# Optimization experiments

Measured on AMD Instinct MI355X. Metric: run time of the kernel, lower is better.

Reference implementation:

```python
import jax, jax.numpy as jnp
import numpy as np
from jax import lax

B, H, W = 4096, 15, 15
P, V = 16, 32
D = P + V            # 48
PCODE = 2380
NEMB = 2 * (PCODE + 1)  # 4762


def _conv(x, w, b=None, groups=1, pad='SAME'):
    # x: [B,C,H,W], w: [O, I/groups, kh, kw] (torch OIHW layout)
    y = lax.conv_general_dilated(
        x, w, window_strides=(1, 1), padding=pad,
        dimension_numbers=('NCHW', 'OIHW', 'NCHW'),
        feature_group_count=groups)
    if b is not None:
        y = y + b[None, :, None, None]
    return y


def setup_inputs() -> dict:
    key = jax.random.key(0)
    ks = jax.random.split(key, 18)
    f = lambda k, shape: (jax.random.normal(k, shape, jnp.float32) * 0.05)
    inp = {
        'emb': f(ks[0], (NEMB, D)),
        'conv_w': f(ks[1], (D, 1, 3, 3)),      # depthwise, groups=D
        'conv_b': f(ks[2], (D,)),
        'ppw_w': f(ks[3], (P, P, 1, 1)),
        'ppw_b': f(ks[4], (P,)),
        'pdw_w': f(ks[5], (P, 1, 3, 3)),       # depthwise, groups=P
        'pdw_b': f(ks[6], (P,)),
        'pf_w': f(ks[7], (1, P, 1, 1)),        # final policy conv, no bias
        'vpw_w': f(ks[8], (V, V, 1, 1)),
        'vpw_b': f(ks[9], (V,)),
        'vl1_w': f(ks[10], (V, V)),
        'vl1_b': f(ks[11], (V,)),
        'vl2_w': f(ks[12], (V, V)),
        'vl2_b': f(ks[13], (V,)),
        'vf_w': f(ks[14], (3, V)),
        'vf_b': f(ks[15], (3,)),
        'sparse_feature_input': jax.random.randint(ks[16], (B, 12, H, W), 0, PCODE, jnp.int32),
        'board_input': jax.random.randint(ks[17], (B, 2, H, W), 0, 2, jnp.int32),
    }
    return inp


def reference(emb, conv_w, conv_b, ppw_w, ppw_b, pdw_w, pdw_b, pf_w,
              vpw_w, vpw_b, vl1_w, vl1_b, vl2_w, vl2_b, vf_w, vf_b,
              sparse_feature_input, board_input):
    relu = jax.nn.relu
    # --- PatternCodeEmbedding ---
    pcode = sparse_feature_input[:, 10:12]                     # [B,2,H,W]
    pcode = jnp.where(board_input > 0, PCODE, pcode)
    pcode = pcode + jnp.array([0, PCODE + 1], jnp.int32)[None, :, None, None]
    feat = emb[pcode].sum(axis=1)                              # [B,H,W,D]
    feat = jnp.transpose(feat, (0, 3, 1, 2))                   # [B,D,H,W]
    # --- trunk depthwise conv ---
    feat = relu(_conv(feat, conv_w, conv_b, groups=D))
    # --- policy head ---
    pol = feat[:, :P]
    pol = relu(_conv(pol, ppw_w, ppw_b))
    pol = relu(_conv(pol, pdw_w, pdw_b, groups=P))
    pol = _conv(pol, pf_w)                                     # [B,1,H,W]
    # --- value head ---
    val = feat[:, P:]
    val = relu(_conv(val, vpw_w, vpw_b))
    val = jnp.mean(val, axis=(2, 3))                           # [B,V]
    val = relu(val @ vl1_w.T + vl1_b)
    val = relu(val @ vl2_w.T + vl2_b)
    val = val @ vf_w.T + vf_b                                  # [B,3]
    return val, pol
```

## Files before the change

kernel.cpp:

```cpp
#include <hip/hip_runtime.h>
#include <hip/hip_fp16.h>

typedef _Float16 half8  __attribute__((ext_vector_type(8)));
typedef _Float16 half4_t __attribute__((ext_vector_type(4)));
typedef _Float16 half2_t __attribute__((ext_vector_type(2)));
typedef float f32x4 __attribute__((ext_vector_type(4)));

namespace {
constexpr int NT = 256;
constexpr int NPIX = 225;
constexpr int PCODE_C = 2380;

constexpr int OFF_A     = 0;
constexpr int OFF_X     = 25200;
constexpr int OFF_WC    = 48240;
constexpr int OFF_WCB   = 49104;
constexpr int OFF_WPD   = 49200;
constexpr int OFF_WPDB  = 49488;
constexpr int OFF_SV    = 49520;
constexpr int OFF_H1    = 49648;
constexpr int OFF_H2    = 49776;
constexpr int SMEM_BYTES = 49904;

constexpr int OFF_POLA  = 0;
constexpr int OFF_POLB  = 10800;
}

__device__ __forceinline__ void wave_fence() {
    asm volatile("s_waitcnt lgkmcnt(0)" ::: "memory");
}

__global__ __launch_bounds__(NT) void patnet_kernel(
    const float* __restrict__ emb,
    const float* __restrict__ conv_w, const float* __restrict__ conv_b,
    const float* __restrict__ ppw_w,  const float* __restrict__ ppw_b,
    const float* __restrict__ pdw_w,  const float* __restrict__ pdw_b,
    const float* __restrict__ pf_w,
    const float* __restrict__ vpw_w,  const float* __restrict__ vpw_b,
    const float* __restrict__ vl1_w,  const float* __restrict__ vl1_b,
    const float* __restrict__ vl2_w,  const float* __restrict__ vl2_b,
    const float* __restrict__ vf_w,   const float* __restrict__ vf_b,
    const int* __restrict__ sparse,   const int* __restrict__ board,
    float* __restrict__ out, int batch)
{
    __shared__ __align__(16) unsigned char smem[SMEM_BYTES];
    const int tid  = threadIdx.x;
    const int b    = blockIdx.x;
    const int lane = tid & 63;
    const int wave = tid >> 6;

    int c0 = 0, c1 = 0;
    if (tid < NPIX) {
        int s10 = sparse[b * 2700 + 10 * NPIX + tid];
        int s11 = sparse[b * 2700 + 11 * NPIX + tid];
        int b0  = board[b * 450 + tid];
        int b1  = board[b * 450 + NPIX + tid];
        c0 = (b0 > 0) ? PCODE_C : s10;
        c1 = ((b1 > 0) ? PCODE_C : s11) + (PCODE_C + 1);
    }

    {
        _Float16* Wc   = (_Float16*)(smem + OFF_WC);
        _Float16* Wcb  = (_Float16*)(smem + OFF_WCB);
        _Float16* Wpd  = (_Float16*)(smem + OFF_WPD);
        _Float16* Wpdb = (_Float16*)(smem + OFF_WPDB);
        for (int i = tid; i < 432; i += NT) {
            int cg = i / 72, rem = i - cg * 72;
            int t = rem >> 3, j = rem & 7;
            Wc[i] = (_Float16)conv_w[(cg * 8 + j) * 9 + t];
        }
        for (int i = tid; i < 48; i += NT) Wcb[i] = (_Float16)conv_b[i];
        for (int i = tid; i < 144; i += NT) {
            int cg = i / 72, rem = i - cg * 72;
            int t = rem >> 3, j = rem & 7;
            Wpd[i] = (_Float16)pdw_w[(cg * 8 + j) * 9 + t];
        }
        for (int i = tid; i < 16; i += NT) Wpdb[i] = (_Float16)pdw_b[i];
    }

    if (tid < NPIX) {
        const float* e0 = emb + c0 * 48;
        const float* e1 = emb + c1 * 48;
        #pragma unroll
        for (int g = 0; g < 6; g++) {
            f32x4 x0 = *(const f32x4*)(e0 + g * 8);
            f32x4 x1 = *(const f32x4*)(e0 + g * 8 + 4);
            f32x4 y0 = *(const f32x4*)(e1 + g * 8);
            f32x4 y1 = *(const f32x4*)(e1 + g * 8 + 4);
            f32x4 s0 = x0 + y0, s1 = x1 + y1;
            half8 hv = {(_Float16)s0.x, (_Float16)s0.y, (_Float16)s0.z, (_Float16)s0.w,
                        (_Float16)s1.x, (_Float16)s1.y, (_Float16)s1.z, (_Float16)s1.w};
            *(half8*)(smem + OFF_A + tid * 112 + g * 16) = hv;
        }
    }
    __syncthreads();

    if (tid < 252) {
        int cg = tid % 6, prow = tid / 6;
        const _Float16* wb = (const _Float16*)(smem + OFF_WC) + cg * 72;
        half8 wv[9];
        #pragma unroll
        for (int t = 0; t < 9; t++) wv[t] = *(const half8*)(wb + t * 8);
        half8 bias = *(const half8*)((const _Float16*)(smem + OFF_WCB) + cg * 8);
        for (int p = prow; p < NPIX; p += 42) {
            int y = p / 15, x = p - y * 15;
            half8 acc = bias;
            #pragma unroll
            for (int dy = -1; dy <= 1; dy++) {
                int yy = y + dy;
                if ((unsigned)yy >= 15u) continue;
                #pragma unroll
                for (int dx = -1; dx <= 1; dx++) {
                    int xx = x + dx;
                    if ((unsigned)xx >= 15u) continue;
                    half8 v = *(const half8*)(smem + OFF_A + (yy * 15 + xx) * 112 + cg * 16);
                    acc = __builtin_elementwise_fma(v, wv[(dy + 1) * 3 + (dx + 1)], acc);
                }
            }
            acc = __builtin_elementwise_max(acc, (half8)(_Float16)0.f);
            *(half8*)(smem + OFF_X + p * 96 + cg * 16) = acc;
        }
    }
    __syncthreads();

    const int n = lane & 15, q = lane >> 4;

    if (wave < 3) {
        half8 af;
        {
            const float* wp = ppw_w + n * 16 + (q & 1) * 8;
            f32x4 w0 = *(const f32x4*)wp;
            f32x4 w1 = *(const f32x4*)(wp + 4);
            half8 t = {(_Float16)w0.x, (_Float16)w0.y, (_Float16)w0.z, (_Float16)w0.w,
                       (_Float16)w1.x, (_Float16)w1.y, (_Float16)w1.z, (_Float16)w1.w};
            af = (q < 2) ? t : (half8)(_Float16)0.f;
        }
        f32x4 pb = *(const f32x4*)(ppw_b + q * 4);
        const int tlo = (wave == 0) ? 0 : ((wave == 1) ? 3 : 8);
        const int thi = (wave == 0) ? 6 : ((wave == 1) ? 11 : 15);
        for (int t = tlo; t < thi; t++) {
            int p = t * 16 + n;
            half8 bf = *(const half8*)(smem + OFF_X + p * 96 + q * 16);
            f32x4 d = __builtin_amdgcn_mfma_f32_16x16x32_f16(af, bf, (f32x4)(0.f), 0, 0, 0);
            if (p < NPIX) {
                half4_t hv = {(_Float16)fmaxf(d.x + pb.x, 0.f),
                              (_Float16)fmaxf(d.y + pb.y, 0.f),
                              (_Float16)fmaxf(d.z + pb.z, 0.f),
                              (_Float16)fmaxf(d.w + pb.w, 0.f)};
                *(half4_t*)(smem + OFF_POLA + p * 48 + q * 8) = hv;
            }
        }
        wave_fence();

        const int px0 = wave * 75;
        {
            int cg = lane & 1;
            const _Float16* wb = (const _Float16*)(smem + OFF_WPD) + cg * 72;
            half8 wv[9];
            #pragma unroll
            for (int t = 0; t < 9; t++) wv[t] = *(const half8*)(wb + t * 8);
            half8 bias = *(const half8*)((const _Float16*)(smem + OFF_WPDB) + cg * 8);
            for (int i = 0; i < 3; i++) {
                int idx = i * 64 + lane;
                if (idx < 150) {
                    int px = px0 + (idx >> 1);
                    int y = px / 15, x = px - y * 15;
                    half8 acc = bias;
                    #pragma unroll
                    for (int dy = -1; dy <= 1; dy++) {
                        int yy = y + dy;
                        if ((unsigned)yy >= 15u) continue;
                        #pragma unroll
                        for (int dx = -1; dx <= 1; dx++) {
                            int xx = x + dx;
                            if ((unsigned)xx >= 15u) continue;
                            half8 v = *(const half8*)(smem + OFF_POLA + (yy * 15 + xx) * 48 + cg * 16);
                            acc = __builtin_elementwise_fma(v, wv[(dy + 1) * 3 + (dx + 1)], acc);
                        }
                    }
                    acc = __builtin_elementwise_max(acc, (half8)(_Float16)0.f);
                    *(half8*)(smem + OFF_POLB + px * 32 + cg * 16) = acc;
                }
            }
        }
        wave_fence();

        {
            half2_t pf[8];
            #pragma unroll
            for (int j = 0; j < 8; j++)
                pf[j] = half2_t{(_Float16)pf_w[2 * j], (_Float16)pf_w[2 * j + 1]};
            for (int i = 0; i < 2; i++) {
                int off = i * 64 + lane;
                if (off < 75) {
                    int px = px0 + off;
                    half8 u0 = *(const half8*)(smem + OFF_POLB + px * 32);
                    half8 u1 = *(const half8*)(smem + OFF_POLB + px * 32 + 16);
                    float acc = 0.f;
                    acc = __builtin_amdgcn_fdot2(half2_t{u0[0], u0[1]}, pf[0], acc, false);
                    acc = __builtin_amdgcn_fdot2(half2_t{u0[2], u0[3]}, pf[1], acc, false);
                    acc = __builtin_amdgcn_fdot2(half2_t{u0[4], u0[5]}, pf[2], acc, false);
                    acc = __builtin_amdgcn_fdot2(half2_t{u0[6], u0[7]}, pf[3], acc, false);
                    acc = __builtin_amdgcn_fdot2(half2_t{u1[0], u1[1]}, pf[4], acc, false);
                    acc = __builtin_amdgcn_fdot2(half2_t{u1[2], u1[3]}, pf[5], acc, false);
                    acc = __builtin_amdgcn_fdot2(half2_t{u1[4], u1[5]}, pf[6], acc, false);
                    acc = __builtin_amdgcn_fdot2(half2_t{u1[6], u1[7]}, pf[7], acc, false);
                    out[3 * batch + b * NPIX + px] = acc;
                }
            }
        }
    } else {
        half8 af0, af1;
        {
            const float* wp = vpw_w + n * 32 + q * 8;
            f32x4 w0 = *(const f32x4*)wp, w1 = *(const f32x4*)(wp + 4);
            af0 = half8{(_Float16)w0.x, (_Float16)w0.y, (_Float16)w0.z, (_Float16)w0.w,
                        (_Float16)w1.x, (_Float16)w1.y, (_Float16)w1.z, (_Float16)w1.w};
            const float* wp2 = vpw_w + (16 + n) * 32 + q * 8;
            f32x4 v0 = *(const f32x4*)wp2, v1 = *(const f32x4*)(wp2 + 4);
            af1 = half8{(_Float16)v0.x, (_Float16)v0.y, (_Float16)v0.z, (_Float16)v0.w,
                        (_Float16)v1.x, (_Float16)v1.y, (_Float16)v1.z, (_Float16)v1.w};
        }
        f32x4 vb0 = *(const f32x4*)(vpw_b + q * 4);
        f32x4 vb1 = *(const f32x4*)(vpw_b + 16 + q * 4);
        f32x4 a0 = {0.f, 0.f, 0.f, 0.f}, a1 = {0.f, 0.f, 0.f, 0.f};
        for (int t = 0; t < 15; t++) {
            int p = t * 16 + n;
            half8 bf = *(const half8*)(smem + OFF_X + p * 96 + 32 + q * 16);
            f32x4 d0 = __builtin_amdgcn_mfma_f32_16x16x32_f16(af0, bf, (f32x4)(0.f), 0, 0, 0);
            f32x4 d1 = __builtin_amdgcn_mfma_f32_16x16x32_f16(af1, bf, (f32x4)(0.f), 0, 0, 0);
            if (p < NPIX) {
                #pragma unroll
                for (int r = 0; r < 4; r++) {
                    a0[r] += fmaxf(d0[r] + vb0[r], 0.f);
                    a1[r] += fmaxf(d1[r] + vb1[r], 0.f);
                }
            }
        }
        #pragma unroll
        for (int s = 1; s < 16; s <<= 1) {
            #pragma unroll
            for (int r = 0; r < 4; r++) {
                a0[r] += __shfl_xor(a0[r], s, 64);
                a1[r] += __shfl_xor(a1[r], s, 64);
            }
        }
        if (n == 0) {
            f32x4 m0 = a0 * (1.f / 225.f), m1 = a1 * (1.f / 225.f);
            *(f32x4*)(smem + OFF_SV + q * 16) = m0;
            *(f32x4*)(smem + OFF_SV + 64 + q * 16) = m1;
        }
        wave_fence();

        int o = lane & 31;
        float acc1 = vl1_b[o];
        #pragma unroll
        for (int g = 0; g < 8; g++) {
            f32x4 sv = *(const f32x4*)(smem + OFF_SV + g * 16);
            f32x4 w4 = *(const f32x4*)(vl1_w + o * 32 + g * 4);
            acc1 += sv.x * w4.x + sv.y * w4.y + sv.z * w4.z + sv.w * w4.w;
        }
        acc1 = fmaxf(acc1, 0.f);
        if (lane < 32) *(float*)(smem + OFF_H1 + o * 4) = acc1;
        wave_fence();

        float acc2 = vl2_b[o];
        #pragma unroll
        for (int g = 0; g < 8; g++) {
            f32x4 hv = *(const f32x4*)(smem + OFF_H1 + g * 16);
            f32x4 w4 = *(const f32x4*)(vl2_w + o * 32 + g * 4);
            acc2 += hv.x * w4.x + hv.y * w4.y + hv.z * w4.z + hv.w * w4.w;
        }
        acc2 = fmaxf(acc2, 0.f);
        if (lane < 32) *(float*)(smem + OFF_H2 + o * 4) = acc2;
        wave_fence();

        if (lane < 3) {
            float acc3 = vf_b[lane];
            #pragma unroll
            for (int g = 0; g < 8; g++) {
                f32x4 hv = *(const f32x4*)(smem + OFF_H2 + g * 16);
                f32x4 w4 = *(const f32x4*)(vf_w + lane * 32 + g * 4);
                acc3 += hv.x * w4.x + hv.y * w4.y + hv.z * w4.z + hv.w * w4.w;
            }
            out[b * 3 + lane] = acc3;
        }
    }
}

extern "C" void kernel_launch(void* const* d_in, const int* in_sizes, int n_in,
                              void* d_out, int out_size, void* d_ws, size_t ws_size,
                              hipStream_t stream) {
    const float* emb    = (const float*)d_in[0];
    const float* conv_w = (const float*)d_in[1];
    const float* conv_b = (const float*)d_in[2];
    const float* ppw_w  = (const float*)d_in[3];
    const float* ppw_b  = (const float*)d_in[4];
    const float* pdw_w  = (const float*)d_in[5];
    const float* pdw_b  = (const float*)d_in[6];
    const float* pf_w   = (const float*)d_in[7];
    const float* vpw_w  = (const float*)d_in[8];
    const float* vpw_b  = (const float*)d_in[9];
    const float* vl1_w  = (const float*)d_in[10];
    const float* vl1_b  = (const float*)d_in[11];
    const float* vl2_w  = (const float*)d_in[12];
    const float* vl2_b  = (const float*)d_in[13];
    const float* vf_w   = (const float*)d_in[14];
    const float* vf_b   = (const float*)d_in[15];
    const int* sparse   = (const int*)d_in[16];
    const int* board    = (const int*)d_in[17];
    float* out = (float*)d_out;

    int batch = in_sizes[16] / 2700;
    patnet_kernel<<<batch, NT, 0, stream>>>(
        emb, conv_w, conv_b, ppw_w, ppw_b, pdw_w, pdw_b, pf_w,
        vpw_w, vpw_b, vl1_w, vl1_b, vl2_w, vl2_b, vf_w, vf_b,
        sparse, board, out, batch);
}
```

Before: 178.4 us.

## Use zero-padded channel-group-major LDS layout and strip-based depthwise convolutions

```diff
diff --git a/kernel.cpp b/kernel.cpp
--- a/kernel.cpp
+++ b/kernel.cpp
@@ -4,6 +4,7 @@
 typedef _Float16 half8  __attribute__((ext_vector_type(8)));
 typedef _Float16 half4_t __attribute__((ext_vector_type(4)));
 typedef _Float16 half2_t __attribute__((ext_vector_type(2)));
+typedef __fp16   fp16x2  __attribute__((ext_vector_type(2)));
 typedef float f32x4 __attribute__((ext_vector_type(4)));
 
 namespace {
@@ -11,26 +12,31 @@
 constexpr int NPIX = 225;
 constexpr int PCODE_C = 2380;
 
+constexpr int APITCH_Y  = 272;
+constexpr int APITCH_CG = 4624;
+
 constexpr int OFF_A     = 0;
-constexpr int OFF_X     = 25200;
-constexpr int OFF_WC    = 48240;
-constexpr int OFF_WCB   = 49104;
-constexpr int OFF_WPD   = 49200;
-constexpr int OFF_WPDB  = 49488;
-constexpr int OFF_SV    = 49520;
-constexpr int OFF_H1    = 49648;
-constexpr int OFF_H2    = 49776;
-constexpr int SMEM_BYTES = 49904;
+constexpr int OFF_X     = 27744;
+constexpr int OFF_WC    = 50784;
+constexpr int OFF_WCB   = 51648;
+constexpr int OFF_WPD   = 51744;
+constexpr int OFF_WPDB  = 52032;
+constexpr int OFF_SV    = 52064;
+constexpr int OFF_H1    = 52192;
+constexpr int OFF_H2    = 52320;
+constexpr int SMEM_BYTES = 52448;
 
 constexpr int OFF_POLA  = 0;
-constexpr int OFF_POLB  = 10800;
-}
-
+}
+
+__device__ __forceinline__ half2_t pkrtz(float a, float b) {
+    return __builtin_bit_cast(half2_t, __builtin_amdgcn_cvt_pkrtz(a, b));
+}
 __device__ __forceinline__ void wave_fence() {
     asm volatile("s_waitcnt lgkmcnt(0)" ::: "memory");
 }
 
-__global__ __launch_bounds__(NT) void patnet_kernel(
+__global__ __launch_bounds__(NT, 3) void patnet_kernel(
     const float* __restrict__ emb,
     const float* __restrict__ conv_w, const float* __restrict__ conv_b,
     const float* __restrict__ ppw_w,  const float* __restrict__ ppw_b,
@@ -76,11 +82,21 @@
             Wpd[i] = (_Float16)pdw_w[(cg * 8 + j) * 9 + t];
         }
         for (int i = tid; i < 16; i += NT) Wpdb[i] = (_Float16)pdw_b[i];
+        for (int i = tid; i < 384; i += NT) {
+            int cg = i >> 6, j = i & 63;
+            int row, col;
+            if (j < 17)      { row = 0;  col = j; }
+            else if (j < 34) { row = 16; col = j - 17; }
+            else { int k = j - 34; row = 1 + (k >> 1); col = (k & 1) * 16; }
+            *(half8*)(smem + OFF_A + cg * APITCH_CG + row * APITCH_Y + col * 16) = (half8)(_Float16)0.f;
+        }
     }
 
     if (tid < NPIX) {
         const float* e0 = emb + c0 * 48;
         const float* e1 = emb + c1 * 48;
+        int y = tid / 15, x = tid - y * 15;
+        unsigned char* abase = smem + OFF_A + (y + 1) * APITCH_Y + (x + 1) * 16;
         #pragma unroll
         for (int g = 0; g < 6; g++) {
             f32x4 x0 = *(const f32x4*)(e0 + g * 8);
@@ -88,141 +104,138 @@
             f32x4 y0 = *(const f32x4*)(e1 + g * 8);
             f32x4 y1 = *(const f32x4*)(e1 + g * 8 + 4);
             f32x4 s0 = x0 + y0, s1 = x1 + y1;
-            half8 hv = {(_Float16)s0.x, (_Float16)s0.y, (_Float16)s0.z, (_Float16)s0.w,
-                        (_Float16)s1.x, (_Float16)s1.y, (_Float16)s1.z, (_Float16)s1.w};
-            *(half8*)(smem + OFF_A + tid * 112 + g * 16) = hv;
+            half2_t q0 = pkrtz(s0.x, s0.y), q1 = pkrtz(s0.z, s0.w);
+            half2_t q2 = pkrtz(s1.x, s1.y), q3 = pkrtz(s1.z, s1.w);
+            half8 hv = {q0[0], q0[1], q1[0], q1[1], q2[0], q2[1], q3[0], q3[1]};
+            *(half8*)(abase + g * APITCH_CG) = hv;
         }
     }
     __syncthreads();
 
-    if (tid < 252) {
-        int cg = tid % 6, prow = tid / 6;
-        const _Float16* wb = (const _Float16*)(smem + OFF_WC) + cg * 72;
+    auto do_strip = [&](int t) {
+        int cg = t / 45, rem = t - cg * 45;
+        int y = rem / 3, s = rem - y * 3;
+        int xs = s * 5;
+        const unsigned char* wb = smem + OFF_WC + cg * 144;
         half8 wv[9];
         #pragma unroll
-        for (int t = 0; t < 9; t++) wv[t] = *(const half8*)(wb + t * 8);
-        half8 bias = *(const half8*)((const _Float16*)(smem + OFF_WCB) + cg * 8);
-        for (int p = prow; p < NPIX; p += 42) {
-            int y = p / 15, x = p - y * 15;
-            half8 acc = bias;
+        for (int i = 0; i < 9; i++) wv[i] = *(const half8*)(wb + i * 16);
+        half8 bias = *(const half8*)(smem + OFF_WCB + cg * 16);
+        half8 acc[5] = {bias, bias, bias, bias, bias};
+        const unsigned char* ab = smem + OFF_A + cg * APITCH_CG + y * APITCH_Y + xs * 16;
+        #pragma unroll
+        for (int c = 0; c < 7; c++) {
+            half8 v0 = *(const half8*)(ab + c * 16);
+            half8 v1 = *(const half8*)(ab + APITCH_Y + c * 16);
+            half8 v2 = *(const half8*)(ab + 2 * APITCH_Y + c * 16);
             #pragma unroll
-            for (int dy = -1; dy <= 1; dy++) {
-                int yy = y + dy;
-                if ((unsigned)yy >= 15u) continue;
-                #pragma unroll
-                for (int dx = -1; dx <= 1; dx++) {
-                    int xx = x + dx;
-                    if ((unsigned)xx >= 15u) continue;
-                    half8 v = *(const half8*)(smem + OFF_A + (yy * 15 + xx) * 112 + cg * 16);
-                    acc = __builtin_elementwise_fma(v, wv[(dy + 1) * 3 + (dx + 1)], acc);
+            for (int o = 0; o < 5; o++) {
+                int kx = c - o;
+                if (kx >= 0 && kx <= 2) {
+                    acc[o] = __builtin_elementwise_fma(v0, wv[kx],     acc[o]);
+                    acc[o] = __builtin_elementwise_fma(v1, wv[3 + kx], acc[o]);
+                    acc[o] = __builtin_elementwise_fma(v2, wv[6 + kx], acc[o]);
                 }
             }
-            acc = __builtin_elementwise_max(acc, (half8)(_Float16)0.f);
-            *(half8*)(smem + OFF_X + p * 96 + cg * 16) = acc;
-        }
-    }
+        }
+        unsigned char* xw = smem + OFF_X + (y * 15 + xs) * 96 + cg * 16;
+        #pragma unroll
+        for (int o = 0; o < 5; o++)
+            *(half8*)(xw + o * 96) = __builtin_elementwise_max(acc[o], (half8)(_Float16)0.f);
+    };
+    do_strip(tid);
+    {
+        int e = wave * 4 + lane;
+        if (lane < 4 && e < 14) do_strip(256 + e);
+    }
+
+    const int n = lane & 15, q = lane >> 4;
+    half8 af_p;
+    {
+        const float* wp = ppw_w + n * 16 + (q & 1) * 8;
+        f32x4 w0 = *(const f32x4*)wp, w1 = *(const f32x4*)(wp + 4);
+        half8 t = {(_Float16)w0.x, (_Float16)w0.y, (_Float16)w0.z, (_Float16)w0.w,
+                   (_Float16)w1.x, (_Float16)w1.y, (_Float16)w1.z, (_Float16)w1.w};
+        af_p = (q < 2) ? t : (half8)(_Float16)0.f;
+    }
+    f32x4 pb = *(const f32x4*)(ppw_b + q * 4);
+    half2_t pfh[8];
+    #pragma unroll
+    for (int j = 0; j < 8; j++) pfh[j] = pkrtz(pf_w[2 * j], pf_w[2 * j + 1]);
+    half8 af0, af1;
+    {
+        const float* wp = vpw_w + n * 32 + q * 8;
+        f32x4 w0 = *(const f32x4*)wp, w1 = *(const f32x4*)(wp + 4);
+        af0 = half8{(_Float16)w0.x, (_Float16)w0.y, (_Float16)w0.z, (_Float16)w0.w,
+                    (_Float16)w1.x, (_Float16)w1.y, (_Float16)w1.z, (_Float16)w1.w};
+        const float* wp2 = vpw_w + (16 + n) * 32 + q * 8;
+        f32x4 v0 = *(const f32x4*)wp2, v1 = *(const f32x4*)(wp2 + 4);
+        af1 = half8{(_Float16)v0.x, (_Float16)v0.y, (_Float16)v0.z, (_Float16)v0.w,
+                    (_Float16)v1.x, (_Float16)v1.y, (_Float16)v1.z, (_Float16)v1.w};
+    }
+    f32x4 vb0 = *(const f32x4*)(vpw_b + q * 4);
+    f32x4 vb1 = *(const f32x4*)(vpw_b + 16 + q * 4);
     __syncthreads();
 
-    const int n = lane & 15, q = lane >> 4;
-
     if (wave < 3) {
-        half8 af;
-        {
-            const float* wp = ppw_w + n * 16 + (q & 1) * 8;
-            f32x4 w0 = *(const f32x4*)wp;
-            f32x4 w1 = *(const f32x4*)(wp + 4);
-            half8 t = {(_Float16)w0.x, (_Float16)w0.y, (_Float16)w0.z, (_Float16)w0.w,
-                       (_Float16)w1.x, (_Float16)w1.y, (_Float16)w1.z, (_Float16)w1.w};
-            af = (q < 2) ? t : (half8)(_Float16)0.f;
-        }
-        f32x4 pb = *(const f32x4*)(ppw_b + q * 4);
+        #pragma unroll
+        for (int i0 = 0; i0 < 2; i0++) {
+            int i = i0 * 64 + lane;
+            int cg = i >> 6, j = i & 63;
+            int row, col;
+            if (j < 17)      { row = 0;  col = j; }
+            else if (j < 34) { row = 16; col = j - 17; }
+            else { int k = j - 34; row = 1 + (k >> 1); col = (k & 1) * 16; }
+            *(half8*)(smem + OFF_POLA + cg * APITCH_CG + row * APITCH_Y + col * 16) = (half8)(_Float16)0.f;
+        }
+        const int cgp = lane & 1;
+        half8 wvp[9];
+        #pragma unroll
+        for (int t = 0; t < 9; t++) wvp[t] = *(const half8*)(smem + OFF_WPD + cgp * 144 + t * 16);
+        half8 biasp = *(const half8*)(smem + OFF_WPDB + cgp * 16);
+
         const int tlo = (wave == 0) ? 0 : ((wave == 1) ? 3 : 8);
         const int thi = (wave == 0) ? 6 : ((wave == 1) ? 11 : 15);
+        const int cg3 = q >> 1;
         for (int t = tlo; t < thi; t++) {
             int p = t * 16 + n;
             half8 bf = *(const half8*)(smem + OFF_X + p * 96 + q * 16);
-            f32x4 d = __builtin_amdgcn_mfma_f32_16x16x32_f16(af, bf, (f32x4)(0.f), 0, 0, 0);
+            f32x4 d = __builtin_amdgcn_mfma_f32_16x16x32_f16(af_p, bf, (f32x4)(0.f), 0, 0, 0);
             if (p < NPIX) {
-                half4_t hv = {(_Float16)fmaxf(d.x + pb.x, 0.f),
-                              (_Float16)fmaxf(d.y + pb.y, 0.f),
-                              (_Float16)fmaxf(d.z + pb.z, 0.f),
-                              (_Float16)fmaxf(d.w + pb.w, 0.f)};
-                *(half4_t*)(smem + OFF_POLA + p * 48 + q * 8) = hv;
+                int y = p / 15, x = p - y * 15;
+                half2_t lo = pkrtz(fmaxf(d.x + pb.x, 0.f), fmaxf(d.y + pb.y, 0.f));
+                half2_t hi = pkrtz(fmaxf(d.z + pb.z, 0.f), fmaxf(d.w + pb.w, 0.f));
+                half4_t hv = {lo[0], lo[1], hi[0], hi[1]};
+                *(half4_t*)(smem + OFF_POLA + cg3 * APITCH_CG + (y + 1) * APITCH_Y + (x + 1) * 16 + (q & 1) * 8) = hv;
             }
         }
         wave_fence();
 
         const int px0 = wave * 75;
-        {
-            int cg = lane & 1;
-            const _Float16* wb = (const _Float16*)(smem + OFF_WPD) + cg * 72;
-            half8 wv[9];
-            #pragma unroll
-            for (int t = 0; t < 9; t++) wv[t] = *(const half8*)(wb + t * 8);
-            half8 bias = *(const half8*)((const _Float16*)(smem + OFF_WPDB) + cg * 8);
-            for (int i = 0; i < 3; i++) {
-                int idx = i * 64 + lane;
-                if (idx < 150) {
-                    int px = px0 + (idx >> 1);
-                    int y = px / 15, x = px - y * 15;
-                    half8 acc = bias;
-                    #pragma unroll
-                    for (int dy = -1; dy <= 1; dy++) {
-                        int yy = y + dy;
-                        if ((unsigned)yy >= 15u) continue;
-                        #pragma unroll
-                        for (int dx = -1; dx <= 1; dx++) {
-                            int xx = x + dx;
-                            if ((unsigned)xx >= 15u) continue;
-                            half8 v = *(const half8*)(smem + OFF_POLA + (yy * 15 + xx) * 48 + cg * 16);
-                            acc = __builtin_elementwise_fma(v, wv[(dy + 1) * 3 + (dx + 1)], acc);
-                        }
-                    }
-                    acc = __builtin_elementwise_max(acc, (half8)(_Float16)0.f);
-                    *(half8*)(smem + OFF_POLB + px * 32 + cg * 16) = acc;
+        for (int i = 0; i < 3; i++) {
+            int idx = i * 64 + lane;
+            if (idx < 150) {
+                int px = px0 + (idx >> 1);
+                int y = px / 15, x = px - y * 15;
+                const unsigned char* pbse = smem + OFF_POLA + cgp * APITCH_CG + y * APITCH_Y + x * 16;
+                half8 acc = biasp;
+                #pragma unroll
+                for (int ky = 0; ky < 3; ky++) {
+                    acc = __builtin_elementwise_fma(*(const half8*)(pbse + ky * APITCH_Y),      wvp[ky * 3 + 0], acc);
+                    acc = __builtin_elementwise_fma(*(const half8*)(pbse + ky * APITCH_Y + 16), wvp[ky * 3 + 1], acc);
+                    acc = __builtin_elementwise_fma(*(const half8*)(pbse + ky * APITCH_Y + 32), wvp[ky * 3 + 2], acc);
                 }
-            }
-        }
-        wave_fence();
-
-        {
-            half2_t pf[8];
-            #pragma unroll
-            for (int j = 0; j < 8; j++)
-                pf[j] = half2_t{(_Float16)pf_w[2 * j], (_Float16)pf_w[2 * j + 1]};
-            for (int i = 0; i < 2; i++) {
-                int off = i * 64 + lane;
-                if (off < 75) {
-                    int px = px0 + off;
-                    half8 u0 = *(const half8*)(smem + OFF_POLB + px * 32);
-                    half8 u1 = *(const half8*)(smem + OFF_POLB + px * 32 + 16);
-                    float acc = 0.f;
-                    acc = __builtin_amdgcn_fdot2(half2_t{u0[0], u0[1]}, pf[0], acc, false);
-                    acc = __builtin_amdgcn_fdot2(half2_t{u0[2], u0[3]}, pf[1], acc, false);
-                    acc = __builtin_amdgcn_fdot2(half2_t{u0[4], u0[5]}, pf[2], acc, false);
-                    acc = __builtin_amdgcn_fdot2(half2_t{u0[6], u0[7]}, pf[3], acc, false);
-                    acc = __builtin_amdgcn_fdot2(half2_t{u1[0], u1[1]}, pf[4], acc, false);
-                    acc = __builtin_amdgcn_fdot2(half2_t{u1[2], u1[3]}, pf[5], acc, false);
-                    acc = __builtin_amdgcn_fdot2(half2_t{u1[4], u1[5]}, pf[6], acc, false);
-                    acc = __builtin_amdgcn_fdot2(half2_t{u1[6], u1[7]}, pf[7], acc, false);
-                    out[3 * batch + b * NPIX + px] = acc;
-                }
+                acc = __builtin_elementwise_max(acc, (half8)(_Float16)0.f);
+                float part = 0.f;
+                part = __builtin_amdgcn_fdot2(half2_t{acc[0], acc[1]}, pfh[cgp * 4 + 0], part, false);
+                part = __builtin_amdgcn_fdot2(half2_t{acc[2], acc[3]}, pfh[cgp * 4 + 1], part, false);
+                part = __builtin_amdgcn_fdot2(half2_t{acc[4], acc[5]}, pfh[cgp * 4 + 2], part, false);
+                part = __builtin_amdgcn_fdot2(half2_t{acc[6], acc[7]}, pfh[cgp * 4 + 3], part, false);
+                float tot = part + __shfl_xor(part, 1, 64);
+                if (cgp == 0) out[3 * batch + b * NPIX + px] = tot;
             }
         }
     } else {
-        half8 af0, af1;
-        {
-            const float* wp = vpw_w + n * 32 + q * 8;
-            f32x4 w0 = *(const f32x4*)wp, w1 = *(const f32x4*)(wp + 4);
-            af0 = half8{(_Float16)w0.x, (_Float16)w0.y, (_Float16)w0.z, (_Float16)w0.w,
-                        (_Float16)w1.x, (_Float16)w1.y, (_Float16)w1.z, (_Float16)w1.w};
-            const float* wp2 = vpw_w + (16 + n) * 32 + q * 8;
-            f32x4 v0 = *(const f32x4*)wp2, v1 = *(const f32x4*)(wp2 + 4);
-            af1 = half8{(_Float16)v0.x, (_Float16)v0.y, (_Float16)v0.z, (_Float16)v0.w,
-                        (_Float16)v1.x, (_Float16)v1.y, (_Float16)v1.z, (_Float16)v1.w};
-        }
-        f32x4 vb0 = *(const f32x4*)(vpw_b + q * 4);
-        f32x4 vb1 = *(const f32x4*)(vpw_b + 16 + q * 4);
         f32x4 a0 = {0.f, 0.f, 0.f, 0.f}, a1 = {0.f, 0.f, 0.f, 0.f};
         for (int t = 0; t < 15; t++) {
             int p = t * 16 + n;
@@ -246,42 +259,49 @@
             }
         }
         if (n == 0) {
-            f32x4 m0 = a0 * (1.f / 225.f), m1 = a1 * (1.f / 225.f);
-            *(f32x4*)(smem + OFF_SV + q * 16) = m0;
-            *(f32x4*)(smem + OFF_SV + 64 + q * 16) = m1;
+            *(f32x4*)(smem + OFF_SV + q * 16)      = a0 * (1.f / 225.f);
+            *(f32x4*)(smem + OFF_SV + 64 + q * 16) = a1 * (1.f / 225.f);
+        }
+        const int o = lane & 31;
+        f32x4 w1r[8], w2r[8], w3r[8];
+        float b1v = vl1_b[o], b2v = vl2_b[o], b3v = 0.f;
+        #pragma unroll
+        for (int g = 0; g < 8; g++) w1r[g] = *(const f32x4*)(vl1_w + o * 32 + g * 4);
+        #pragma unroll
+        for (int g = 0; g < 8; g++) w2r[g] = *(const f32x4*)(vl2_w + o * 32 + g * 4);
+        if (lane < 3) {
+            b3v = vf_b[lane];
+            #pragma unroll
+            for (int g = 0; g < 8; g++) w3r[g] = *(const f32x4*)(vf_w + lane * 32 + g * 4);
         }
         wave_fence();
 
-        int o = lane & 31;
-        float acc1 = vl1_b[o];
+        float acc1 = b1v;
         #pragma unroll
         for (int g = 0; g < 8; g++) {
             f32x4 sv = *(const f32x4*)(smem + OFF_SV + g * 16);
-            f32x4 w4 = *(const f32x4*)(vl1_w + o * 32 + g * 4);
-            acc1 += sv.x * w4.x + sv.y * w4.y + sv.z * w4.z + sv.w * w4.w;
+            acc1 += sv.x * w1r[g].x + sv.y * w1r[g].y + sv.z * w1r[g].z + sv.w * w1r[g].w;
         }
         acc1 = fmaxf(acc1, 0.f);
         if (lane < 32) *(float*)(smem + OFF_H1 + o * 4) = acc1;
         wave_fence();
 
-        float acc2 = vl2_b[o];
+        float acc2 = b2v;
         #pragma unroll
         for (int g = 0; g < 8; g++) {
             f32x4 hv = *(const f32x4*)(smem + OFF_H1 + g * 16);
-            f32x4 w4 = *(const f32x4*)(vl2_w + o * 32 + g * 4);
-            acc2 += hv.x * w4.x + hv.y * w4.y + hv.z * w4.z + hv.w * w4.w;
+            acc2 += hv.x * w2r[g].x + hv.y * w2r[g].y + hv.z * w2r[g].z + hv.w * w2r[g].w;
         }
         acc2 = fmaxf(acc2, 0.f);
         if (lane < 32) *(float*)(smem + OFF_H2 + o * 4) = acc2;
         wave_fence();
 
         if (lane < 3) {
-            float acc3 = vf_b[lane];
+            float acc3 = b3v;
             #pragma unroll
             for (int g = 0; g < 8; g++) {
                 f32x4 hv = *(const f32x4*)(smem + OFF_H2 + g * 16);
-                f32x4 w4 = *(const f32x4*)(vf_w + lane * 32 + g * 4);
-                acc3 += hv.x * w4.x + hv.y * w4.y + hv.z * w4.z + hv.w * w4.w;
+                acc3 += hv.x * w3r[g].x + hv.y * w3r[g].y + hv.z * w3r[g].z + hv.w * w3r[g].w;
             }
             out[b * 3 + lane] = acc3;
         }
```

After: 174.4 us. -2.2%, faster.
